# Optimization experiments

Measured on AMD Instinct MI355X. Metric: run time of the kernel, lower is better.

## Reference

```python
import jax, jax.numpy as jnp
import numpy as np

B = 4096   # batch
I = 1024   # in_features
O = 1024   # out_features
N = 4      # LUT fan-in; table size 2**N = 16


def setup_inputs() -> dict:
    key = jax.random.key(0)
    k1, k2, k3 = jax.random.split(key, 3)
    return {
        "x": jax.random.normal(k1, (B, I), dtype=jnp.float32),
        # learnable mapping logits: (out_features, n, in_features)
        "mapping_logits": jax.random.normal(k2, (O, N, I), dtype=jnp.float32),
        # per-node LUT tables with 2**n corner values each
        "lut_tables": jax.random.normal(k3, (O, 2 ** N), dtype=jnp.float32),
    }


def reference(x, mapping_logits, lut_tables):
    # softmax-weighted input selection: (B,I) x (O,N,I) -> (B,O,N)
    w = jax.nn.softmax(mapping_logits, axis=-1)
    selected = jnp.einsum('bi,oni->bon', x, w)
    # BatchedLUTNodes: squash to [0,1], multilinear interpolation over 2**N corners
    s = jax.nn.sigmoid(selected)                      # (B,O,N)
    cw = jnp.ones(s.shape[:2] + (1,), dtype=s.dtype)  # corner weights, grows to (B,O,2**N)
    for j in range(N):                                # fixed small loop over fan-in
        sj = s[..., j][..., None]                     # (B,O,1)
        cw = jnp.concatenate([cw * (1.0 - sj), cw * sj], axis=-1)
    # weighted sum of per-node table entries -> (B,O)
    return jnp.einsum('boc,oc->bo', cw, lut_tables)
```

## Files before the change

kernel.cpp:

```cpp
#include <hip/hip_runtime.h>

#define B_DIM 4096
#define I_DIM 1024
#define O_DIM 1024
#define ON_DIM 4096
#define TILE_HALFS 4096

typedef _Float16 half8  __attribute__((ext_vector_type(8)));
typedef _Float16 half4_t __attribute__((ext_vector_type(4)));
typedef float    floatx4 __attribute__((ext_vector_type(4)));

__global__ __launch_bounds__(256)
void ltn_stats(const float* __restrict__ logits, float2* __restrict__ stats) {
  const int t = threadIdx.x, lane = t & 63, wv = t >> 6;
  const int row = blockIdx.x * 4 + wv;
  const float4* src = (const float4*)(logits + (size_t)row * I_DIM);
  float4 v[4];
#pragma unroll
  for (int j = 0; j < 4; j++) v[j] = src[j * 64 + lane];
  float m = -1e30f;
#pragma unroll
  for (int j = 0; j < 4; j++)
    m = fmaxf(m, fmaxf(fmaxf(v[j].x, v[j].y), fmaxf(v[j].z, v[j].w)));
#pragma unroll
  for (int off = 1; off < 64; off <<= 1) m = fmaxf(m, __shfl_xor(m, off));
  float s = 0.0f;
#pragma unroll
  for (int j = 0; j < 4; j++) {
    s += __expf(v[j].x - m) + __expf(v[j].y - m)
       + __expf(v[j].z - m) + __expf(v[j].w - m);
  }
#pragma unroll
  for (int off = 1; off < 64; off <<= 1) s += __shfl_xor(s, off);
  if (lane == 0) stats[row] = make_float2(m, 1.0f / s);
}

__global__ __launch_bounds__(256)
void ltn_tile(const float* __restrict__ logits, const float* __restrict__ x,
              const float2* __restrict__ stats,
              _Float16* __restrict__ wt, _Float16* __restrict__ xt) {
  const int t  = threadIdx.x;
  const int nn = t >> 1;
  const int hf = t & 1;
  if (blockIdx.x < 1024) {
    const int nb = blockIdx.x >> 5, kb = blockIdx.x & 31;
    const int row = nb * 128 + nn;
    const float2 st = stats[row];
    const float4* src = (const float4*)(logits + (size_t)row * I_DIM + kb * 32 + hf * 16);
    const float4 a = src[0], b = src[1], c = src[2], d = src[3];
    half8 h0, h1;
    h0[0] = (_Float16)(__expf(a.x - st.x) * st.y);
    h0[1] = (_Float16)(__expf(a.y - st.x) * st.y);
    h0[2] = (_Float16)(__expf(a.z - st.x) * st.y);
    h0[3] = (_Float16)(__expf(a.w - st.x) * st.y);
    h0[4] = (_Float16)(__expf(b.x - st.x) * st.y);
    h0[5] = (_Float16)(__expf(b.y - st.x) * st.y);
    h0[6] = (_Float16)(__expf(b.z - st.x) * st.y);
    h0[7] = (_Float16)(__expf(b.w - st.x) * st.y);
    h1[0] = (_Float16)(__expf(c.x - st.x) * st.y);
    h1[1] = (_Float16)(__expf(c.y - st.x) * st.y);
    h1[2] = (_Float16)(__expf(c.z - st.x) * st.y);
    h1[3] = (_Float16)(__expf(c.w - st.x) * st.y);
    h1[4] = (_Float16)(__expf(d.x - st.x) * st.y);
    h1[5] = (_Float16)(__expf(d.y - st.x) * st.y);
    h1[6] = (_Float16)(__expf(d.z - st.x) * st.y);
    h1[7] = (_Float16)(__expf(d.w - st.x) * st.y);
    _Float16* base = wt + ((size_t)nb * 32 + kb) * TILE_HALFS + (hf * 2) * 1024 + nn * 8;
    *(half8*)base = h0;
    *(half8*)(base + 1024) = h1;
  } else {
    const int bid = blockIdx.x - 1024;
    const int mb = bid >> 5, kt = bid & 31;
    const int row = mb * 128 + nn;
    const float4* src = (const float4*)(x + (size_t)row * I_DIM + kt * 32 + hf * 16);
    const float4 a = src[0], b = src[1], c = src[2], d = src[3];
    half8 h0, h1;
    h0[0] = (_Float16)a.x; h0[1] = (_Float16)a.y; h0[2] = (_Float16)a.z; h0[3] = (_Float16)a.w;
    h0[4] = (_Float16)b.x; h0[5] = (_Float16)b.y; h0[6] = (_Float16)b.z; h0[7] = (_Float16)b.w;
    h1[0] = (_Float16)c.x; h1[1] = (_Float16)c.y; h1[2] = (_Float16)c.z; h1[3] = (_Float16)c.w;
    h1[4] = (_Float16)d.x; h1[5] = (_Float16)d.y; h1[6] = (_Float16)d.z; h1[7] = (_Float16)d.w;
    _Float16* base = xt + ((size_t)mb * 32 + kt) * TILE_HALFS + (hf * 2) * 1024 + nn * 8;
    *(half8*)base = h0;
    *(half8*)(base + 1024) = h1;
  }
}

__global__ __launch_bounds__(512, 2)
void ltn_gemm_lut(const _Float16* __restrict__ xt,
                  const _Float16* __restrict__ wt,
                  const float* __restrict__ lut,
                  float* __restrict__ out) {
  __shared__ _Float16 As[2][2][4][128][8];
  __shared__ _Float16 Bs[2][2][4][128][8];

  const int tid  = threadIdx.x;
  const int lane = tid & 63;
  const int wv   = tid >> 6;
  const int wr   = wv >> 1;
  const int wc   = wv & 1;
  const int mb   = blockIdx.x;
  const int nb   = blockIdx.y;
  const int fm   = lane & 15;
  const int kq   = lane >> 4;

  const size_t baseA = (size_t)(mb * 2) * 32 * TILE_HALFS;
  const size_t baseB = (size_t)(nb * 2) * 32 * TILE_HALFS;

  floatx4 acc[4][8];
#pragma unroll
  for (int i = 0; i < 4; i++)
#pragma unroll
    for (int j = 0; j < 8; j++) acc[i][j] = (floatx4)0.0f;

  auto stage = [&](int buf, int kt) {
#pragma unroll
    for (int s = 0; s < 4; s++) {
      const int c   = wv * 4 + s;
      const int cc  = c & 15;
      const int tl  = cc >> 3;
      const int sub = cc & 7;
      const _Float16* g;
      char* l;
      if (c < 16) {
        g = xt + baseA + (size_t)(tl * 32 + kt) * TILE_HALFS + sub * 512 + lane * 8;
        l = (char*)&As[buf][0][0][0][0] + cc * 1024;
      } else {
        g = wt + baseB + (size_t)(tl * 32 + kt) * TILE_HALFS + sub * 512 + lane * 8;
        l = (char*)&Bs[buf][0][0][0][0] + cc * 1024;
      }
      __builtin_amdgcn_global_load_lds(
          (const __attribute__((address_space(1))) void*)g,
          (__attribute__((address_space(3))) void*)l, 16, 0, 0);
    }
  };

  auto compute = [&](int buf) {
    half8 af[4], bf[8];
#pragma unroll
    for (int f = 0; f < 4; f++)
      af[f] = *(const half8*)&As[buf][wr >> 1][kq][(wr & 1) * 64 + f * 16 + fm][0];
#pragma unroll
    for (int g = 0; g < 8; g++)
      bf[g] = *(const half8*)&Bs[buf][wc][kq][g * 16 + fm][0];
#pragma unroll
    for (int mt = 0; mt < 4; mt++)
#pragma unroll
      for (int nt = 0; nt < 8; nt++)
        acc[mt][nt] = __builtin_amdgcn_mfma_f32_16x16x32_f16(
            af[mt], bf[nt], acc[mt][nt], 0, 0, 0);
  };

  stage(0, 0);
  int buf = 0;
  for (int kt = 0; kt < 32; kt++) {
    __syncthreads();
    if (kt + 1 < 32) stage(buf ^ 1, kt + 1);
    compute(buf);
    buf ^= 1;
  }

#pragma unroll
  for (int nt = 0; nt < 8; nt++) {
    const int o = (nb * 256 + wc * 128 + nt * 16 + fm) >> 2;
    const float4* lt4 = (const float4*)(lut + (size_t)o * 16);
    const float4 L0 = lt4[0], L1 = lt4[1], L2 = lt4[2], L3 = lt4[3];
#pragma unroll
    for (int mt = 0; mt < 4; mt++) {
#pragma unroll
      for (int r = 0; r < 4; r++) {
        const float v  = acc[mt][nt][r];
        const float sv = 1.0f / (1.0f + __expf(-v));
        const float s1 = __shfl_down(sv, 1);
        const float s2 = __shfl_down(sv, 2);
        const float s3 = __shfl_down(sv, 3);
        if ((lane & 3) == 0) {
          const float s0 = sv;
          const float a0 = L0.x + (L2.x - L0.x) * s3;
          const float a1 = L0.y + (L2.y - L0.y) * s3;
          const float a2 = L0.z + (L2.z - L0.z) * s3;
          const float a3 = L0.w + (L2.w - L0.w) * s3;
          const float a4 = L1.x + (L3.x - L1.x) * s3;
          const float a5 = L1.y + (L3.y - L1.y) * s3;
          const float a6 = L1.z + (L3.z - L1.z) * s3;
          const float a7 = L1.w + (L3.w - L1.w) * s3;
          const float b0 = a0 + (a4 - a0) * s2;
          const float b1 = a1 + (a5 - a1) * s2;
          const float b2 = a2 + (a6 - a2) * s2;
          const float b3 = a3 + (a7 - a3) * s2;
          const float c0 = b0 + (b2 - b0) * s1;
          const float c1 = b1 + (b3 - b1) * s1;
          const float res = c0 + (c1 - c0) * s0;
          const int row = mb * 256 + wr * 64 + mt * 16 + (lane >> 4) * 4 + r;
          out[(size_t)row * O_DIM + o] = res;
        }
      }
    }
  }
}

extern "C" void kernel_launch(void* const* d_in, const int* in_sizes, int n_in,
                              void* d_out, int out_size, void* d_ws, size_t ws_size,
                              hipStream_t stream) {
  const float* x      = (const float*)d_in[0];
  const float* logits = (const float*)d_in[1];
  const float* lut    = (const float*)d_in[2];
  float* out          = (float*)d_out;

  _Float16* wt = (_Float16*)d_ws;
  _Float16* xt = (_Float16*)d_ws + (size_t)ON_DIM * I_DIM;
  float2* stats = (float2*)d_out;

  ltn_stats<<<1024, 256, 0, stream>>>(logits, stats);
  ltn_tile<<<2048, 256, 0, stream>>>(logits, x, stats, wt, xt);
  dim3 grid(16, 16);
  ltn_gemm_lut<<<grid, 512, 0, stream>>>(xt, wt, lut, out);
}
```

Measured before the change: 133.7 us.

## Switch GEMM to 32x32x16 MFMA with 256x128 tiles and fold x-cast into stats pass

```diff
diff --git a/kernel.cpp b/kernel.cpp
--- a/kernel.cpp
+++ b/kernel.cpp
@@ -6,71 +6,40 @@
 #define ON_DIM 4096
 #define TILE_HALFS 4096
 
-typedef _Float16 half8  __attribute__((ext_vector_type(8)));
+typedef _Float16 half8   __attribute__((ext_vector_type(8)));
 typedef _Float16 half4_t __attribute__((ext_vector_type(4)));
-typedef float    floatx4 __attribute__((ext_vector_type(4)));
+typedef float    floatx16 __attribute__((ext_vector_type(16)));
 
 __global__ __launch_bounds__(256)
-void ltn_stats(const float* __restrict__ logits, float2* __restrict__ stats) {
-  const int t = threadIdx.x, lane = t & 63, wv = t >> 6;
-  const int row = blockIdx.x * 4 + wv;
-  const float4* src = (const float4*)(logits + (size_t)row * I_DIM);
-  float4 v[4];
-#pragma unroll
-  for (int j = 0; j < 4; j++) v[j] = src[j * 64 + lane];
-  float m = -1e30f;
-#pragma unroll
-  for (int j = 0; j < 4; j++)
-    m = fmaxf(m, fmaxf(fmaxf(v[j].x, v[j].y), fmaxf(v[j].z, v[j].w)));
-#pragma unroll
-  for (int off = 1; off < 64; off <<= 1) m = fmaxf(m, __shfl_xor(m, off));
-  float s = 0.0f;
-#pragma unroll
-  for (int j = 0; j < 4; j++) {
-    s += __expf(v[j].x - m) + __expf(v[j].y - m)
-       + __expf(v[j].z - m) + __expf(v[j].w - m);
-  }
-#pragma unroll
-  for (int off = 1; off < 64; off <<= 1) s += __shfl_xor(s, off);
-  if (lane == 0) stats[row] = make_float2(m, 1.0f / s);
-}
-
-__global__ __launch_bounds__(256)
-void ltn_tile(const float* __restrict__ logits, const float* __restrict__ x,
-              const float2* __restrict__ stats,
-              _Float16* __restrict__ wt, _Float16* __restrict__ xt) {
-  const int t  = threadIdx.x;
-  const int nn = t >> 1;
-  const int hf = t & 1;
+void ltn_prep1(const float* __restrict__ logits, const float* __restrict__ x,
+               float2* __restrict__ stats, _Float16* __restrict__ xt) {
+  const int t = threadIdx.x;
   if (blockIdx.x < 1024) {
-    const int nb = blockIdx.x >> 5, kb = blockIdx.x & 31;
-    const int row = nb * 128 + nn;
-    const float2 st = stats[row];
-    const float4* src = (const float4*)(logits + (size_t)row * I_DIM + kb * 32 + hf * 16);
-    const float4 a = src[0], b = src[1], c = src[2], d = src[3];
-    half8 h0, h1;
-    h0[0] = (_Float16)(__expf(a.x - st.x) * st.y);
-    h0[1] = (_Float16)(__expf(a.y - st.x) * st.y);
-    h0[2] = (_Float16)(__expf(a.z - st.x) * st.y);
-    h0[3] = (_Float16)(__expf(a.w - st.x) * st.y);
-    h0[4] = (_Float16)(__expf(b.x - st.x) * st.y);
-    h0[5] = (_Float16)(__expf(b.y - st.x) * st.y);
-    h0[6] = (_Float16)(__expf(b.z - st.x) * st.y);
-    h0[7] = (_Float16)(__expf(b.w - st.x) * st.y);
-    h1[0] = (_Float16)(__expf(c.x - st.x) * st.y);
-    h1[1] = (_Float16)(__expf(c.y - st.x) * st.y);
-    h1[2] = (_Float16)(__expf(c.z - st.x) * st.y);
-    h1[3] = (_Float16)(__expf(c.w - st.x) * st.y);
-    h1[4] = (_Float16)(__expf(d.x - st.x) * st.y);
-    h1[5] = (_Float16)(__expf(d.y - st.x) * st.y);
-    h1[6] = (_Float16)(__expf(d.z - st.x) * st.y);
-    h1[7] = (_Float16)(__expf(d.w - st.x) * st.y);
-    _Float16* base = wt + ((size_t)nb * 32 + kb) * TILE_HALFS + (hf * 2) * 1024 + nn * 8;
-    *(half8*)base = h0;
-    *(half8*)(base + 1024) = h1;
+    const int lane = t & 63, wv = t >> 6;
+    const int row = blockIdx.x * 4 + wv;
+    const float4* src = (const float4*)(logits + (size_t)row * I_DIM);
+    float4 v[4];
+#pragma unroll
+    for (int j = 0; j < 4; j++) v[j] = src[j * 64 + lane];
+    float m = -1e30f;
+#pragma unroll
+    for (int j = 0; j < 4; j++)
+      m = fmaxf(m, fmaxf(fmaxf(v[j].x, v[j].y), fmaxf(v[j].z, v[j].w)));
+#pragma unroll
+    for (int off = 1; off < 64; off <<= 1) m = fmaxf(m, __shfl_xor(m, off));
+    float s = 0.0f;
+#pragma unroll
+    for (int j = 0; j < 4; j++) {
+      s += __expf(v[j].x - m) + __expf(v[j].y - m)
+         + __expf(v[j].z - m) + __expf(v[j].w - m);
+    }
+#pragma unroll
+    for (int off = 1; off < 64; off <<= 1) s += __shfl_xor(s, off);
+    if (lane == 0) stats[row] = make_float2(m, 1.0f / s);
   } else {
     const int bid = blockIdx.x - 1024;
     const int mb = bid >> 5, kt = bid & 31;
+    const int nn = t >> 1, hf = t & 1;
     const int row = mb * 128 + nn;
     const float4* src = (const float4*)(x + (size_t)row * I_DIM + kt * 32 + hf * 16);
     const float4 a = src[0], b = src[1], c = src[2], d = src[3];
@@ -85,13 +54,45 @@
   }
 }
 
-__global__ __launch_bounds__(512, 2)
+__global__ __launch_bounds__(256)
+void ltn_prep2(const float* __restrict__ logits, const float2* __restrict__ stats,
+               _Float16* __restrict__ wt) {
+  const int t  = threadIdx.x;
+  const int nn = t >> 1, hf = t & 1;
+  const int nb = blockIdx.x >> 5, kb = blockIdx.x & 31;
+  const int row = nb * 128 + nn;
+  const float2 st = stats[row];
+  const float4* src = (const float4*)(logits + (size_t)row * I_DIM + kb * 32 + hf * 16);
+  const float4 a = src[0], b = src[1], c = src[2], d = src[3];
+  half8 h0, h1;
+  h0[0] = (_Float16)(__expf(a.x - st.x) * st.y);
+  h0[1] = (_Float16)(__expf(a.y - st.x) * st.y);
+  h0[2] = (_Float16)(__expf(a.z - st.x) * st.y);
+  h0[3] = (_Float16)(__expf(a.w - st.x) * st.y);
+  h0[4] = (_Float16)(__expf(b.x - st.x) * st.y);
+  h0[5] = (_Float16)(__expf(b.y - st.x) * st.y);
+  h0[6] = (_Float16)(__expf(b.z - st.x) * st.y);
+  h0[7] = (_Float16)(__expf(b.w - st.x) * st.y);
+  h1[0] = (_Float16)(__expf(c.x - st.x) * st.y);
+  h1[1] = (_Float16)(__expf(c.y - st.x) * st.y);
+  h1[2] = (_Float16)(__expf(c.z - st.x) * st.y);
+  h1[3] = (_Float16)(__expf(c.w - st.x) * st.y);
+  h1[4] = (_Float16)(__expf(d.x - st.x) * st.y);
+  h1[5] = (_Float16)(__expf(d.y - st.x) * st.y);
+  h1[6] = (_Float16)(__expf(d.z - st.x) * st.y);
+  h1[7] = (_Float16)(__expf(d.w - st.x) * st.y);
+  _Float16* base = wt + ((size_t)nb * 32 + kb) * TILE_HALFS + (hf * 2) * 1024 + nn * 8;
+  *(half8*)base = h0;
+  *(half8*)(base + 1024) = h1;
+}
+
+__global__ __launch_bounds__(512, 4)
 void ltn_gemm_lut(const _Float16* __restrict__ xt,
                   const _Float16* __restrict__ wt,
                   const float* __restrict__ lut,
                   float* __restrict__ out) {
   __shared__ _Float16 As[2][2][4][128][8];
-  __shared__ _Float16 Bs[2][2][4][128][8];
+  __shared__ _Float16 Bs[2][4][128][8];
 
   const int tid  = threadIdx.x;
   const int lane = tid & 63;
@@ -100,33 +101,32 @@
   const int wc   = wv & 1;
   const int mb   = blockIdx.x;
   const int nb   = blockIdx.y;
-  const int fm   = lane & 15;
-  const int kq   = lane >> 4;
+  const int l31  = lane & 31;
+  const int lhi  = lane >> 5;
 
   const size_t baseA = (size_t)(mb * 2) * 32 * TILE_HALFS;
-  const size_t baseB = (size_t)(nb * 2) * 32 * TILE_HALFS;
-
-  floatx4 acc[4][8];
-#pragma unroll
-  for (int i = 0; i < 4; i++)
-#pragma unroll
-    for (int j = 0; j < 8; j++) acc[i][j] = (floatx4)0.0f;
+  const size_t baseB = (size_t)nb * 32 * TILE_HALFS;
+
+  floatx16 acc[2][2];
+#pragma unroll
+  for (int i = 0; i < 2; i++)
+#pragma unroll
+    for (int j = 0; j < 2; j++) acc[i][j] = (floatx16)0.0f;
 
   auto stage = [&](int buf, int kt) {
 #pragma unroll
-    for (int s = 0; s < 4; s++) {
-      const int c   = wv * 4 + s;
-      const int cc  = c & 15;
-      const int tl  = cc >> 3;
-      const int sub = cc & 7;
+    for (int s = 0; s < 3; s++) {
+      const int c = wv * 3 + s;
       const _Float16* g;
       char* l;
       if (c < 16) {
+        const int tl = c >> 3, sub = c & 7;
         g = xt + baseA + (size_t)(tl * 32 + kt) * TILE_HALFS + sub * 512 + lane * 8;
-        l = (char*)&As[buf][0][0][0][0] + cc * 1024;
+        l = (char*)&As[buf][0][0][0][0] + c * 1024;
       } else {
-        g = wt + baseB + (size_t)(tl * 32 + kt) * TILE_HALFS + sub * 512 + lane * 8;
-        l = (char*)&Bs[buf][0][0][0][0] + cc * 1024;
+        const int sub = c - 16;
+        g = wt + baseB + (size_t)kt * TILE_HALFS + sub * 512 + lane * 8;
+        l = (char*)&Bs[buf][0][0][0] + sub * 1024;
       }
       __builtin_amdgcn_global_load_lds(
           (const __attribute__((address_space(1))) void*)g,
@@ -135,19 +135,25 @@
   };
 
   auto compute = [&](int buf) {
-    half8 af[4], bf[8];
-#pragma unroll
-    for (int f = 0; f < 4; f++)
-      af[f] = *(const half8*)&As[buf][wr >> 1][kq][(wr & 1) * 64 + f * 16 + fm][0];
-#pragma unroll
-    for (int g = 0; g < 8; g++)
-      bf[g] = *(const half8*)&Bs[buf][wc][kq][g * 16 + fm][0];
-#pragma unroll
-    for (int mt = 0; mt < 4; mt++)
-#pragma unroll
-      for (int nt = 0; nt < 8; nt++)
-        acc[mt][nt] = __builtin_amdgcn_mfma_f32_16x16x32_f16(
-            af[mt], bf[nt], acc[mt][nt], 0, 0, 0);
+#pragma unroll
+    for (int s = 0; s < 2; s++) {
+      const int kb = s * 2 + lhi;
+      half8 af[2], bf[2];
+#pragma unroll
+      for (int tm = 0; tm < 2; tm++) {
+        const int rr = wr * 2 + tm;
+        af[tm] = *(const half8*)&As[buf][rr >> 2][kb][(rr & 3) * 32 + l31][0];
+      }
+#pragma unroll
+      for (int tn = 0; tn < 2; tn++)
+        bf[tn] = *(const half8*)&Bs[buf][kb][wc * 64 + tn * 32 + l31][0];
+#pragma unroll
+      for (int tm = 0; tm < 2; tm++)
+#pragma unroll
+        for (int tn = 0; tn < 2; tn++)
+          acc[tm][tn] = __builtin_amdgcn_mfma_f32_32x32x16_f16(
+              af[tm], bf[tn], acc[tm][tn], 0, 0, 0);
+    }
   };
 
   stage(0, 0);
@@ -160,15 +166,15 @@
   }
 
 #pragma unroll
-  for (int nt = 0; nt < 8; nt++) {
-    const int o = (nb * 256 + wc * 128 + nt * 16 + fm) >> 2;
+  for (int tn = 0; tn < 2; tn++) {
+    const int o = (nb * 128 + wc * 64 + tn * 32 + l31) >> 2;
     const float4* lt4 = (const float4*)(lut + (size_t)o * 16);
     const float4 L0 = lt4[0], L1 = lt4[1], L2 = lt4[2], L3 = lt4[3];
 #pragma unroll
-    for (int mt = 0; mt < 4; mt++) {
-#pragma unroll
-      for (int r = 0; r < 4; r++) {
-        const float v  = acc[mt][nt][r];
+    for (int tm = 0; tm < 2; tm++) {
+#pragma unroll
+      for (int r = 0; r < 16; r++) {
+        const float v  = acc[tm][tn][r];
         const float sv = 1.0f / (1.0f + __expf(-v));
         const float s1 = __shfl_down(sv, 1);
         const float s2 = __shfl_down(sv, 2);
@@ -190,7 +196,8 @@
           const float c0 = b0 + (b2 - b0) * s1;
           const float c1 = b1 + (b3 - b1) * s1;
           const float res = c0 + (c1 - c0) * s0;
-          const int row = mb * 256 + wr * 64 + mt * 16 + (lane >> 4) * 4 + r;
+          const int row = mb * 256 + wr * 64 + tm * 32
+                        + (r & 3) + 8 * (r >> 2) + 4 * lhi;
           out[(size_t)row * O_DIM + o] = res;
         }
       }
@@ -210,8 +217,8 @@
   _Float16* xt = (_Float16*)d_ws + (size_t)ON_DIM * I_DIM;
   float2* stats = (float2*)d_out;
 
-  ltn_stats<<<1024, 256, 0, stream>>>(logits, stats);
-  ltn_tile<<<2048, 256, 0, stream>>>(logits, x, stats, wt, xt);
-  dim3 grid(16, 16);
+  ltn_prep1<<<2048, 256, 0, stream>>>(logits, x, stats, xt);
+  ltn_prep2<<<1024, 256, 0, stream>>>(logits, stats, wt);
+  dim3 grid(16, 32);
   ltn_gemm_lut<<<grid, 512, 0, stream>>>(xt, wt, lut, out);
 }
```

After: 138.6 us. 3.7% more time.
